# Performance work log

Measured on AMD Instinct MI355X. Metric: run time of the kernel, lower is better.

## Reference

```python
import jax, jax.numpy as jnp
import numpy as np

TEMPERATURE = 0.7
TOP_P = 0.9
TOP_K = 50
B, V = 128, 128000


def setup_inputs() -> dict:
    key = jax.random.key(0)
    k1, k2, k3 = jax.random.split(key, 3)
    logits = jax.random.normal(k1, (B, V), dtype=jnp.float32) * 3.0
    input_ids = jax.random.randint(k2, (B, 64), 0, V, dtype=jnp.int64)
    u = jax.random.uniform(k3, (B,), dtype=jnp.float32)
    return {"logits": logits, "input_ids": input_ids, "u": u}


def _warp_logits(logits):
    # TemperatureLogitsWarper
    x = logits / TEMPERATURE
    # TopPLogitsWarper (HF semantics): ascending sort, cumulative softmax,
    # remove tokens whose cumulative prob <= 1 - top_p; keep >= 1 token.
    order = jnp.argsort(x, axis=-1)                       # ascending
    sorted_x = jnp.take_along_axis(x, order, axis=-1)
    cum = jnp.cumsum(jax.nn.softmax(sorted_x, axis=-1), axis=-1)
    remove_sorted = cum <= (1.0 - TOP_P)
    remove_sorted = remove_sorted.at[..., -1:].set(False)  # min_tokens_to_keep=1
    inv = jnp.argsort(order, axis=-1)                     # inverse permutation
    remove = jnp.take_along_axis(remove_sorted, inv, axis=-1)
    x = jnp.where(remove, -jnp.inf, x)
    # TopKLogitsWarper: keep top_k, mask everything strictly below the k-th value
    kth = jax.lax.top_k(x, TOP_K)[0][..., -1:]
    x = jnp.where(x < kth, -jnp.inf, x)
    return x


def reference(logits, input_ids, u):
    # input_ids is unused in the warp path (repetition_penalty == 1.0)
    x = _warp_logits(logits)
    probs = jax.nn.softmax(x, axis=-1)                    # [B, V]
    # torch.multinomial(probs, 1) via inverse-CDF with uniform u
    cdf = jnp.cumsum(probs, axis=-1)
    token = jnp.argmax(cdf >= u[:, None], axis=-1)        # [B]
    return token
```

## Files before the change

kernel.cpp:

```cpp
#include <hip/hip_runtime.h>
#include <cmath>


constexpr int   NSPLIT = 32;
constexpr int   BLK    = 256;
constexpr int   TILE4  = BLK * 4;
constexpr int   NBINS  = 1024;
constexpr int   BPL    = NBINS / 64;
constexpr int   TOPK   = 50;
constexpr float TEMP   = 0.7f;
constexpr float SPANS  = 5.0f;
constexpr float SPANC  = 5.0f;
constexpr int   CAPSEG = 512;
constexpr int   NCAND  = NSPLIT * CAPSEG;
constexpr int   BLK_F  = 256;
constexpr int   NDENSE = 4096;
constexpr int   CAPC   = 128;
constexpr float LOG2E_OVER_T = (float)(1.4426950408889634 / 0.7);

__global__ __launch_bounds__(BLK)
void zmc_kernel(const float* __restrict__ logits,
                float* __restrict__ segmax, float* __restrict__ segz,
                float* __restrict__ cand_v, int* __restrict__ cand_i,
                unsigned int* __restrict__ cnt16,
                int V, int seglen)
{
  const int seg  = blockIdx.x;
  const int row  = blockIdx.y;
  const int tid  = threadIdx.x, lane = tid & 63, wave = tid >> 6;
  const int start = seg * seglen;
  const int len  = (V - start < seglen) ? (V - start) : seglen;

  __shared__ float red[BLK / 64];
  __shared__ float s_bm;
  __shared__ unsigned int s_nf;

  if (len <= 0) {
    if (tid == 0) { segmax[row * NSPLIT + seg] = -INFINITY;
                    segz  [row * NSPLIT + seg] = 0.f;
                    cnt16 [row * NSPLIT + seg] = 0u; }
    return;
  }
  if (tid == 0) s_nf = 0u;

  float* cvout = cand_v + ((size_t)row * NSPLIT + seg) * CAPSEG;
  int*   ciout = cand_i + ((size_t)row * NSPLIT + seg) * CAPSEG;

  const float* __restrict__ base = logits + (size_t)row * V + start;
  const int len4 = len >> 2;
  const int tail = len & 3;
  const float4* b4 = reinterpret_cast<const float4*>(base);

  float mb = -INFINITY;
  float zs = 0.f;
  const int ntiles = (len4 + TILE4 - 1) / TILE4;

  for (int t = 0; t < ntiles; ++t) {
    const int tb = t * TILE4;
    float4 r[4];
    #pragma unroll
    for (int u = 0; u < 4; ++u) {
      int i4 = tb + u * BLK + tid;
      r[u] = (i4 < len4) ? b4[i4]
                         : make_float4(-INFINITY, -INFINITY, -INFINITY, -INFINITY);
    }
    float tm = -INFINITY;
    #pragma unroll
    for (int u = 0; u < 4; ++u)
      tm = fmaxf(tm, fmaxf(fmaxf(r[u].x, r[u].y), fmaxf(r[u].z, r[u].w)));
    #pragma unroll
    for (int off = 32; off >= 1; off >>= 1) tm = fmaxf(tm, __shfl_xor(tm, off, 64));
    if (lane == 0) red[wave] = tm;
    __syncthreads();
    if (tid == 0) {
      float v = red[0];
      for (int w = 1; w < BLK / 64; ++w) v = fmaxf(v, red[w]);
      s_bm = v;
    }
    __syncthreads();
    const float mnew = fmaxf(mb, s_bm);
    if (mnew > mb) zs *= exp2f((mb - mnew) * LOG2E_OVER_T);
    mb = mnew;
    const float lo = mb - SPANS;

    #pragma unroll
    for (int u = 0; u < 4; ++u) {
      const int i4 = tb + u * BLK + tid;
      #pragma unroll
      for (int c = 0; c < 4; ++c) {
        float l = (c == 0) ? r[u].x : (c == 1) ? r[u].y : (c == 2) ? r[u].z : r[u].w;
        zs += exp2f((l - mb) * LOG2E_OVER_T);
        if (l > lo) {
          unsigned int p = atomicAdd(&s_nf, 1u);
          if (p < CAPSEG) { cvout[p] = l; ciout[p] = start + (i4 << 2) + c; }
        }
      }
    }
    if (t + 1 < ntiles) __syncthreads();
  }

  if (tail) {
    __syncthreads();
    const int idx = (len4 << 2) + tid;
    float l = (idx < len) ? base[idx] : -INFINITY;
    float tm = l;
    #pragma unroll
    for (int off = 32; off >= 1; off >>= 1) tm = fmaxf(tm, __shfl_xor(tm, off, 64));
    if (lane == 0) red[wave] = tm;
    __syncthreads();
    if (tid == 0) {
      float v = red[0];
      for (int w = 1; w < BLK / 64; ++w) v = fmaxf(v, red[w]);
      s_bm = v;
    }
    __syncthreads();
    const float mnew = fmaxf(mb, s_bm);
    if (mnew > mb) zs *= exp2f((mb - mnew) * LOG2E_OVER_T);
    mb = mnew;
    zs += exp2f((l - mb) * LOG2E_OVER_T);
    if (l > mb - SPANS) {
      unsigned int p = atomicAdd(&s_nf, 1u);
      if (p < CAPSEG) { cvout[p] = l; ciout[p] = start + idx; }
    }
  }

  #pragma unroll
  for (int off = 32; off >= 1; off >>= 1) zs += __shfl_xor(zs, off, 64);
  if (lane == 0) red[wave] = zs;
  __syncthreads();
  if (tid == 0) {
    float v = red[0];
    for (int w = 1; w < BLK / 64; ++w) v += red[w];
    segz  [row * NSPLIT + seg] = v;
    segmax[row * NSPLIT + seg] = mb;
    unsigned int nf = s_nf;
    cnt16[row * NSPLIT + seg] = (nf > CAPSEG) ? (unsigned)CAPSEG : nf;
  }
}

__global__ __launch_bounds__(BLK_F)
void finish_kernel(const float* __restrict__ segmax, const float* __restrict__ segz,
                   const float* __restrict__ cand_v, const int* __restrict__ cand_i,
                   const unsigned int* __restrict__ cnt16,
                   const float* __restrict__ uvec, int* __restrict__ out)
{
  const int row  = blockIdx.x;
  const int tid  = threadIdx.x;
  const int lane = tid & 63;
  const int wave = tid >> 6;
  const float invT = 1.0f / TEMP;

  __shared__ unsigned int hist[NBINS];
  __shared__ unsigned int chunk[64];
  __shared__ unsigned int cnt_s[NSPLIT];
  __shared__ float s_M, s_Z;
  __shared__ int   s_bstar;
  __shared__ unsigned int s_nd;
  __shared__ unsigned int s_nc;
  __shared__ float dn_v[NDENSE];
  __shared__ int   dn_i[NDENSE];
  __shared__ float fv[CAPC];
  __shared__ int   fi[CAPC];
  __shared__ float ov_[CAPC];
  __shared__ int   oi_[CAPC];
  __shared__ float eo[64];
  __shared__ float o2e[64];
  __shared__ int   o2i[64];
  __shared__ int   s_nk;

  if (tid < NSPLIT) cnt_s[tid] = cnt16[row * NSPLIT + tid];
  for (int i = tid; i < NBINS; i += BLK_F) hist[i] = 0u;
  __syncthreads();

  if (tid < 64) {
    float sm = (lane < NSPLIT) ? segmax[row * NSPLIT + lane] : -INFINITY;
    float m = sm;
    #pragma unroll
    for (int off = 32; off >= 1; off >>= 1) m = fmaxf(m, __shfl_xor(m, off, 64));
    float zt = (lane < NSPLIT) ? segz[row * NSPLIT + lane] * expf((sm - m) * invT) : 0.f;
    #pragma unroll
    for (int off = 32; off >= 1; off >>= 1) zt += __shfl_xor(zt, off, 64);
    if (lane == 0) { s_M = m; s_Z = zt; s_nd = 0u; s_nc = 0u; }
  }
  __syncthreads();

  const float M  = s_M;
  const float lo = M - SPANC;
  const float binscale = (float)NBINS / SPANC;
  const float* cvrow = cand_v + (size_t)row * NCAND;
  const int*   cirow = cand_i + (size_t)row * NCAND;

  for (int sg = wave; sg < NSPLIT; sg += BLK_F / 64) {
    const unsigned int c = cnt_s[sg];
    for (unsigned int i = lane; i < c; i += 64) {
      float v = cvrow[sg * CAPSEG + i];
      if (v > lo) {
        unsigned int d = atomicAdd(&s_nd, 1u);
        if (d < (unsigned)NDENSE) {
          dn_v[d] = v;
          dn_i[d] = cirow[sg * CAPSEG + i];
          int b = (int)((v - lo) * binscale);
          b = (b < 0) ? 0 : ((b > NBINS - 1) ? (NBINS - 1) : b);
          atomicAdd(&hist[b], 1u);
        }
      }
    }
  }
  __syncthreads();
  const int n = ((int)s_nd < NDENSE) ? (int)s_nd : NDENSE;

  if (tid < 64) {
    unsigned int csum = 0;
    const int cb = tid * BPL;
    #pragma unroll
    for (int j = 0; j < BPL; ++j) csum += hist[cb + j];
    chunk[tid] = csum;
  }
  __syncthreads();
  if (tid < 64) {
    unsigned int csum = chunk[tid];
    unsigned int suf = 0;
    for (int l2 = 0; l2 < 64; ++l2) {
      unsigned int c2 = chunk[l2];
      suf += (l2 >= tid) ? c2 : 0u;
    }
    unsigned long long bal = __ballot(suf >= (unsigned)TOPK);
    if (bal == 0ull) {
      if (tid == 0) s_bstar = 0;
    } else {
      int L = 63 - __builtin_clzll(bal);
      if (tid == L) {
        unsigned int running = suf - csum;
        const int cb = tid * BPL;
        unsigned int h[BPL];
        #pragma unroll
        for (int j = 0; j < BPL; ++j) h[j] = hist[cb + j];
        int bsel = cb;
        #pragma unroll
        for (int j = BPL - 1; j >= 0; --j) {
          running += h[j];
          if (running >= (unsigned)TOPK) { bsel = cb + j; break; }
        }
        s_bstar = bsel;
      }
    }
  }
  __syncthreads();

  const int bstar = s_bstar;
  for (int i = tid; i < n; i += BLK_F) {
    float v = dn_v[i];
    int b = (int)((v - lo) * binscale);
    b = (b < 0) ? 0 : ((b > NBINS - 1) ? (NBINS - 1) : b);
    if (b >= bstar) {
      unsigned int p = atomicAdd(&s_nc, 1u);
      if (p < CAPC) { fv[p] = v; fi[p] = dn_i[i]; }
    }
  }
  __syncthreads();

  const int ns = ((int)s_nc < CAPC) ? (int)s_nc : CAPC;
  if (tid < 64) {
    float c0v = (lane < ns)      ? fv[lane]      : 0.f;
    int   c0i = (lane < ns)      ? fi[lane]      : 0;
    float c1v = (lane + 64 < ns) ? fv[lane + 64] : 0.f;
    int   c1i = (lane + 64 < ns) ? fi[lane + 64] : 0;
    int r0 = 0, r1 = 0;
    for (int j = 0; j < ns; ++j) {
      float vj = fv[j]; int ij = fi[j];
      if (vj > c0v || (vj == c0v && ij < c0i)) ++r0;
      if (vj > c1v || (vj == c1v && ij < c1i)) ++r1;
    }
    if (lane < ns)      { ov_[r0] = c0v; oi_[r0] = c0i; }
    if (lane + 64 < ns) { ov_[r1] = c1v; oi_[r1] = c1i; }
  }
  __syncthreads();

  const float Mx = M / TEMP;
  if (tid < 64 && lane < ns && lane < TOPK) {
    float x = ov_[lane] / TEMP;
    eo[lane] = expf(x - Mx);
  }
  __syncthreads();

  if (tid == 0) {
    const float thresh = 0.9f * s_Z;
    const int nkmax = (ns < TOPK) ? ns : TOPK;
    float cum = 0.f; int nk = 0;
    for (int k = 0; k < TOPK; ++k) {
      float ek = eo[k];
      bool take = (k < nkmax) && (cum < thresh);
      if (take) { cum += ek; nk++; }
    }
    s_nk = nk;
  }
  __syncthreads();

  const int nk = s_nk;
  if (tid < 64 && lane < nk) {
    int myi = oi_[lane];
    int rank = 0;
    for (int j = 0; j < nk; ++j) rank += (oi_[j] < myi) ? 1 : 0;
    o2e[rank] = eo[lane]; o2i[rank] = myi;
  }
  __syncthreads();

  if (tid == 0) {
    float S = 0.f;
    for (int j = 0; j < nk; ++j) S += o2e[j];
    const float uu = uvec[row];
    float c = 0.f; int token = 0; int found = 0;
    for (int j = 0; j < nk; ++j) {
      float q = o2e[j] / S;
      c += q;
      if (!found && c >= uu) { token = o2i[j]; found = 1; }
    }
    out[row] = token;
  }
}

extern "C" void kernel_launch(void* const* d_in, const int* in_sizes, int n_in,
                              void* d_out, int out_size, void* d_ws, size_t ws_size,
                              hipStream_t stream) {
  const float* logits = (const float*)d_in[0];
  const float* u = (const float*)d_in[2];
  int* out = (int*)d_out;
  const int B = in_sizes[2];
  const int V = in_sizes[0] / B;
  int seglen = (V + NSPLIT - 1) / NSPLIT;
  seglen = (seglen + 3) & ~3;

  char* ws = (char*)d_ws;
  float* segmax = (float*)ws;
  float* segz   = segmax + (size_t)B * NSPLIT;
  unsigned int* cnt16 = (unsigned int*)(segz + (size_t)B * NSPLIT);
  float* cand_v = (float*)(cnt16 + (size_t)B * NSPLIT);
  int*   cand_i = (int*)(cand_v + (size_t)B * NCAND);

  zmc_kernel<<<dim3(NSPLIT, B), dim3(BLK), 0, stream>>>(
      logits, segmax, segz, cand_v, cand_i, cnt16, V, seglen);
  finish_kernel<<<dim3(B), dim3(BLK_F), 0, stream>>>(
      segmax, segz, cand_v, cand_i, cnt16, u, out);
}
```

Measured before the change: 53.05 us.

## Split max/sum pass from candidate collection using global row max threshold

Replaces the single pass that tracked a running block max with per-tile barriers with two kernels. The first computes per-segment online max and softmax sum with no intra-loop synchronization. The second rereads the logits and collects only values within a span of the global row max, which should yield far fewer candidates, so per-segment capacity and the dense buffer shrink. The cost is a second full read of the logits (about 65MB total, likely partly served from cache) and an extra kernel launch.

```diff
diff --git a/kernel.cpp b/kernel.cpp
--- a/kernel.cpp
+++ b/kernel.cpp
@@ -3,27 +3,24 @@
 
 
 constexpr int   NSPLIT = 32;
+constexpr int   NSEGC  = 64;
 constexpr int   BLK    = 256;
-constexpr int   TILE4  = BLK * 4;
 constexpr int   NBINS  = 1024;
 constexpr int   BPL    = NBINS / 64;
 constexpr int   TOPK   = 50;
 constexpr float TEMP   = 0.7f;
-constexpr float SPANS  = 5.0f;
 constexpr float SPANC  = 5.0f;
-constexpr int   CAPSEG = 512;
-constexpr int   NCAND  = NSPLIT * CAPSEG;
+constexpr int   CAPSG  = 64;
+constexpr int   NCANDC = NSEGC * CAPSG;
 constexpr int   BLK_F  = 256;
-constexpr int   NDENSE = 4096;
+constexpr int   NDENSE = 2048;
 constexpr int   CAPC   = 128;
 constexpr float LOG2E_OVER_T = (float)(1.4426950408889634 / 0.7);
 
 __global__ __launch_bounds__(BLK)
-void zmc_kernel(const float* __restrict__ logits,
-                float* __restrict__ segmax, float* __restrict__ segz,
-                float* __restrict__ cand_v, int* __restrict__ cand_i,
-                unsigned int* __restrict__ cnt16,
-                int V, int seglen)
+void mz_kernel(const float* __restrict__ logits,
+               float* __restrict__ segmax, float* __restrict__ segz,
+               int V, int seglen)
 {
   const int seg  = blockIdx.x;
   const int row  = blockIdx.y;
@@ -31,117 +28,135 @@
   const int start = seg * seglen;
   const int len  = (V - start < seglen) ? (V - start) : seglen;
 
-  __shared__ float red[BLK / 64];
-  __shared__ float s_bm;
-  __shared__ unsigned int s_nf;
+  __shared__ float redm[BLK / 64];
+  __shared__ float redz[BLK / 64];
 
   if (len <= 0) {
     if (tid == 0) { segmax[row * NSPLIT + seg] = -INFINITY;
-                    segz  [row * NSPLIT + seg] = 0.f;
-                    cnt16 [row * NSPLIT + seg] = 0u; }
+                    segz  [row * NSPLIT + seg] = 0.f; }
     return;
   }
-  if (tid == 0) s_nf = 0u;
-
-  float* cvout = cand_v + ((size_t)row * NSPLIT + seg) * CAPSEG;
-  int*   ciout = cand_i + ((size_t)row * NSPLIT + seg) * CAPSEG;
 
   const float* __restrict__ base = logits + (size_t)row * V + start;
   const int len4 = len >> 2;
-  const int tail = len & 3;
   const float4* b4 = reinterpret_cast<const float4*>(base);
-
-  float mb = -INFINITY;
-  float zs = 0.f;
-  const int ntiles = (len4 + TILE4 - 1) / TILE4;
-
-  for (int t = 0; t < ntiles; ++t) {
-    const int tb = t * TILE4;
-    float4 r[4];
-    #pragma unroll
-    for (int u = 0; u < 4; ++u) {
-      int i4 = tb + u * BLK + tid;
-      r[u] = (i4 < len4) ? b4[i4]
-                         : make_float4(-INFINITY, -INFINITY, -INFINITY, -INFINITY);
-    }
-    float tm = -INFINITY;
-    #pragma unroll
-    for (int u = 0; u < 4; ++u)
-      tm = fmaxf(tm, fmaxf(fmaxf(r[u].x, r[u].y), fmaxf(r[u].z, r[u].w)));
-    #pragma unroll
-    for (int off = 32; off >= 1; off >>= 1) tm = fmaxf(tm, __shfl_xor(tm, off, 64));
-    if (lane == 0) red[wave] = tm;
-    __syncthreads();
-    if (tid == 0) {
-      float v = red[0];
-      for (int w = 1; w < BLK / 64; ++w) v = fmaxf(v, red[w]);
-      s_bm = v;
-    }
-    __syncthreads();
-    const float mnew = fmaxf(mb, s_bm);
-    if (mnew > mb) zs *= exp2f((mb - mnew) * LOG2E_OVER_T);
-    mb = mnew;
-    const float lo = mb - SPANS;
-
-    #pragma unroll
-    for (int u = 0; u < 4; ++u) {
-      const int i4 = tb + u * BLK + tid;
+  const float k = LOG2E_OVER_T;
+
+  float tm = -INFINITY;
+  float tz = 0.f;
+
+  for (int i = tid; i < len4; i += BLK) {
+    float4 a = b4[i];
+    float lm = fmaxf(fmaxf(a.x, a.y), fmaxf(a.z, a.w));
+    if (lm > tm) {
+      tz *= exp2f((tm - lm) * k);
+      tm = lm;
+    }
+    float e0 = exp2f((a.x - tm) * k);
+    float e1 = exp2f((a.y - tm) * k);
+    float e2 = exp2f((a.z - tm) * k);
+    float e3 = exp2f((a.w - tm) * k);
+    tz += (e0 + e1) + (e2 + e3);
+  }
+  for (int i = (len4 << 2) + tid; i < len; i += BLK) {
+    float l = base[i];
+    if (l > tm) { tz *= exp2f((tm - l) * k); tm = l; }
+    tz += exp2f((l - tm) * k);
+  }
+
+  #pragma unroll
+  for (int off = 32; off >= 1; off >>= 1) {
+    float om = __shfl_xor(tm, off, 64);
+    float oz = __shfl_xor(tz, off, 64);
+    float mn = fmaxf(tm, om);
+    if (mn > -INFINITY)
+      tz = tz * exp2f((tm - mn) * k) + oz * exp2f((om - mn) * k);
+    else
+      tz = 0.f;
+    tm = mn;
+  }
+  if (lane == 0) { redm[wave] = tm; redz[wave] = tz; }
+  __syncthreads();
+  if (tid == 0) {
+    float m = redm[0], z = redz[0];
+    for (int w = 1; w < BLK / 64; ++w) {
+      float om = redm[w], oz = redz[w];
+      float mn = fmaxf(m, om);
+      if (mn > -INFINITY)
+        z = z * exp2f((m - mn) * k) + oz * exp2f((om - mn) * k);
+      else
+        z = 0.f;
+      m = mn;
+    }
+    segmax[row * NSPLIT + seg] = m;
+    segz  [row * NSPLIT + seg] = z;
+  }
+}
+
+__global__ __launch_bounds__(BLK)
+void collect_kernel(const float* __restrict__ logits,
+                    const float* __restrict__ segmax,
+                    float* __restrict__ cand_v, int* __restrict__ cand_i,
+                    unsigned int* __restrict__ cntc,
+                    int V, int seglen)
+{
+  const int seg  = blockIdx.x;
+  const int row  = blockIdx.y;
+  const int tid  = threadIdx.x, lane = tid & 63;
+  const int start = seg * seglen;
+  const int len  = (V - start < seglen) ? (V - start) : seglen;
+
+  __shared__ unsigned int s_nf;
+
+  if (len <= 0) { if (tid == 0) cntc[row * NSEGC + seg] = 0u; return; }
+
+  float sm = (lane < NSPLIT) ? segmax[row * NSPLIT + lane] : -INFINITY;
+  #pragma unroll
+  for (int off = 32; off >= 1; off >>= 1) sm = fmaxf(sm, __shfl_xor(sm, off, 64));
+  const float lo = sm - SPANC;
+
+  if (tid == 0) s_nf = 0u;
+  __syncthreads();
+
+  float* cvout = cand_v + ((size_t)row * NSEGC + seg) * CAPSG;
+  int*   ciout = cand_i + ((size_t)row * NSEGC + seg) * CAPSG;
+
+  const float* __restrict__ base = logits + (size_t)row * V + start;
+  const int len4 = len >> 2;
+  const float4* b4 = reinterpret_cast<const float4*>(base);
+
+  for (int i = tid; i < len4; i += BLK) {
+    float4 a = b4[i];
+    float lm = fmaxf(fmaxf(a.x, a.y), fmaxf(a.z, a.w));
+    if (lm > lo) {
       #pragma unroll
       for (int c = 0; c < 4; ++c) {
-        float l = (c == 0) ? r[u].x : (c == 1) ? r[u].y : (c == 2) ? r[u].z : r[u].w;
-        zs += exp2f((l - mb) * LOG2E_OVER_T);
+        float l = (c == 0) ? a.x : (c == 1) ? a.y : (c == 2) ? a.z : a.w;
         if (l > lo) {
           unsigned int p = atomicAdd(&s_nf, 1u);
-          if (p < CAPSEG) { cvout[p] = l; ciout[p] = start + (i4 << 2) + c; }
+          if (p < CAPSG) { cvout[p] = l; ciout[p] = start + (i << 2) + c; }
         }
       }
     }
-    if (t + 1 < ntiles) __syncthreads();
-  }
-
-  if (tail) {
-    __syncthreads();
-    const int idx = (len4 << 2) + tid;
-    float l = (idx < len) ? base[idx] : -INFINITY;
-    float tm = l;
-    #pragma unroll
-    for (int off = 32; off >= 1; off >>= 1) tm = fmaxf(tm, __shfl_xor(tm, off, 64));
-    if (lane == 0) red[wave] = tm;
-    __syncthreads();
-    if (tid == 0) {
-      float v = red[0];
-      for (int w = 1; w < BLK / 64; ++w) v = fmaxf(v, red[w]);
-      s_bm = v;
-    }
-    __syncthreads();
-    const float mnew = fmaxf(mb, s_bm);
-    if (mnew > mb) zs *= exp2f((mb - mnew) * LOG2E_OVER_T);
-    mb = mnew;
-    zs += exp2f((l - mb) * LOG2E_OVER_T);
-    if (l > mb - SPANS) {
+  }
+  for (int i = (len4 << 2) + tid; i < len; i += BLK) {
+    float l = base[i];
+    if (l > lo) {
       unsigned int p = atomicAdd(&s_nf, 1u);
-      if (p < CAPSEG) { cvout[p] = l; ciout[p] = start + idx; }
-    }
-  }
-
-  #pragma unroll
-  for (int off = 32; off >= 1; off >>= 1) zs += __shfl_xor(zs, off, 64);
-  if (lane == 0) red[wave] = zs;
+      if (p < CAPSG) { cvout[p] = l; ciout[p] = start + i; }
+    }
+  }
   __syncthreads();
   if (tid == 0) {
-    float v = red[0];
-    for (int w = 1; w < BLK / 64; ++w) v += red[w];
-    segz  [row * NSPLIT + seg] = v;
-    segmax[row * NSPLIT + seg] = mb;
     unsigned int nf = s_nf;
-    cnt16[row * NSPLIT + seg] = (nf > CAPSEG) ? (unsigned)CAPSEG : nf;
+    cntc[row * NSEGC + seg] = (nf > CAPSG) ? (unsigned)CAPSG : nf;
   }
 }
 
 __global__ __launch_bounds__(BLK_F)
 void finish_kernel(const float* __restrict__ segmax, const float* __restrict__ segz,
                    const float* __restrict__ cand_v, const int* __restrict__ cand_i,
-                   const unsigned int* __restrict__ cnt16,
+                   const unsigned int* __restrict__ cntc,
                    const float* __restrict__ uvec, int* __restrict__ out)
 {
   const int row  = blockIdx.x;
@@ -152,7 +167,7 @@
 
   __shared__ unsigned int hist[NBINS];
   __shared__ unsigned int chunk[64];
-  __shared__ unsigned int cnt_s[NSPLIT];
+  __shared__ unsigned int cnt_s[NSEGC];
   __shared__ float s_M, s_Z;
   __shared__ int   s_bstar;
   __shared__ unsigned int s_nd;
@@ -168,7 +183,7 @@
   __shared__ int   o2i[64];
   __shared__ int   s_nk;
 
-  if (tid < NSPLIT) cnt_s[tid] = cnt16[row * NSPLIT + tid];
+  if (tid < NSEGC) cnt_s[tid] = cntc[row * NSEGC + tid];
   for (int i = tid; i < NBINS; i += BLK_F) hist[i] = 0u;
   __syncthreads();
 
@@ -187,18 +202,18 @@
   const float M  = s_M;
   const float lo = M - SPANC;
   const float binscale = (float)NBINS / SPANC;
-  const float* cvrow = cand_v + (size_t)row * NCAND;
-  const int*   cirow = cand_i + (size_t)row * NCAND;
-
-  for (int sg = wave; sg < NSPLIT; sg += BLK_F / 64) {
+  const float* cvrow = cand_v + (size_t)row * NCANDC;
+  const int*   cirow = cand_i + (size_t)row * NCANDC;
+
+  for (int sg = wave; sg < NSEGC; sg += BLK_F / 64) {
     const unsigned int c = cnt_s[sg];
     for (unsigned int i = lane; i < c; i += 64) {
-      float v = cvrow[sg * CAPSEG + i];
+      float v = cvrow[sg * CAPSG + i];
       if (v > lo) {
         unsigned int d = atomicAdd(&s_nd, 1u);
         if (d < (unsigned)NDENSE) {
           dn_v[d] = v;
-          dn_i[d] = cirow[sg * CAPSEG + i];
+          dn_i[d] = cirow[sg * CAPSG + i];
           int b = (int)((v - lo) * binscale);
           b = (b < 0) ? 0 : ((b > NBINS - 1) ? (NBINS - 1) : b);
           atomicAdd(&hist[b], 1u);
@@ -287,9 +302,9 @@
     const float thresh = 0.9f * s_Z;
     const int nkmax = (ns < TOPK) ? ns : TOPK;
     float cum = 0.f; int nk = 0;
-    for (int k = 0; k < TOPK; ++k) {
-      float ek = eo[k];
-      bool take = (k < nkmax) && (cum < thresh);
+    for (int kk = 0; kk < TOPK; ++kk) {
+      float ek = eo[kk];
+      bool take = (kk < nkmax) && (cum < thresh);
       if (take) { cum += ek; nk++; }
     }
     s_nk = nk;
@@ -327,18 +342,20 @@
   int* out = (int*)d_out;
   const int B = in_sizes[2];
   const int V = in_sizes[0] / B;
-  int seglen = (V + NSPLIT - 1) / NSPLIT;
-  seglen = (seglen + 3) & ~3;
+  int seglen1 = (V + NSPLIT - 1) / NSPLIT; seglen1 = (seglen1 + 3) & ~3;
+  int seglenC = (V + NSEGC - 1) / NSEGC;   seglenC = (seglenC + 3) & ~3;
 
   char* ws = (char*)d_ws;
   float* segmax = (float*)ws;
   float* segz   = segmax + (size_t)B * NSPLIT;
-  unsigned int* cnt16 = (unsigned int*)(segz + (size_t)B * NSPLIT);
-  float* cand_v = (float*)(cnt16 + (size_t)B * NSPLIT);
-  int*   cand_i = (int*)(cand_v + (size_t)B * NCAND);
-
-  zmc_kernel<<<dim3(NSPLIT, B), dim3(BLK), 0, stream>>>(
-      logits, segmax, segz, cand_v, cand_i, cnt16, V, seglen);
+  unsigned int* cntc = (unsigned int*)(segz + (size_t)B * NSPLIT);
+  float* cand_v = (float*)(cntc + (size_t)B * NSEGC);
+  int*   cand_i = (int*)(cand_v + (size_t)B * NCANDC);
+
+  mz_kernel<<<dim3(NSPLIT, B), dim3(BLK), 0, stream>>>(
+      logits, segmax, segz, V, seglen1);
+  collect_kernel<<<dim3(NSEGC, B), dim3(BLK), 0, stream>>>(
+      logits, segmax, cand_v, cand_i, cntc, V, seglenC);
   finish_kernel<<<dim3(B), dim3(BLK_F), 0, stream>>>(
-      segmax, segz, cand_v, cand_i, cnt16, u, out);
+      segmax, segz, cand_v, cand_i, cntc, u, out);
 }
```

Result: slower. 57.12 us (+7.7%).
